# Kernel optimization log

Hardware: AMD Instinct MI355X
Metric: run time of the kernel (lower is better)

The kernel has to match this reference:

```python
import jax, jax.numpy as jnp
import numpy as np

D = 85  # label-distribution length -> selects A3 branch

def _build_A(d):
    if d == 5:
        base = jnp.arange(5)
        return 1.0 - jnp.abs(base[:, None] - base[None, :]) / 5.0
    if d == 10:
        base = jnp.arange(10)
        return 1.0 - jnp.abs(base[:, None] - base[None, :]) / 10.0
    base = jnp.arange(85)
    return (1.0 - jnp.abs(base[:, None] - base[None, :]) / 85.0).astype(jnp.float32)

def setup_inputs() -> dict:
    key = jax.random.key(0)
    k1, k2 = jax.random.split(key)
    B = 262144
    inp = jax.random.normal(k1, (B, D), dtype=jnp.float32)
    tgt = jax.random.uniform(k2, (B, D), dtype=jnp.float32)
    return {"input": inp, "target": tgt}

def reference(input, target):
    A = _build_A(input.shape[1]).astype(input.dtype)
    diff = jnp.abs(input - target)            # [B, d]
    # per-row quadratic form diff_i^T A diff_i, summed over batch
    q = jnp.einsum('bi,ij,bj->b', diff, A, diff)
    return 0.1 * q.sum()
```

## Files before the change

kernel.cpp:

```cpp
#include <hip/hip_runtime.h>
#include <hip/hip_bf16.h>


#define QFD_D 85
#define ROWS_PER_BLOCK 128
#define THREADS 256

__global__ __launch_bounds__(THREADS) void qfd_kernel(
    const float* __restrict__ in, const float* __restrict__ tgt,
    float* __restrict__ out) {
    __shared__ float diff[ROWS_PER_BLOCK * QFD_D];
    __shared__ float wsum[THREADS / 64];

    const int tid = threadIdx.x;
    const int E = ROWS_PER_BLOCK * QFD_D;
    const int base = blockIdx.x * E;

    const float4* in4 = reinterpret_cast<const float4*>(in + base);
    const float4* tg4 = reinterpret_cast<const float4*>(tgt + base);
    float4* df4 = reinterpret_cast<float4*>(diff);
    for (int idx = tid; idx < E / 4; idx += THREADS) {
        float4 a = in4[idx];
        float4 b = tg4[idx];
        float4 r;
        r.x = fabsf(a.x - b.x);
        r.y = fabsf(a.y - b.y);
        r.z = fabsf(a.z - b.z);
        r.w = fabsf(a.w - b.w);
        df4[idx] = r;
    }
    __syncthreads();

    float q = 0.0f;
    if (tid < ROWS_PER_BLOCK) {
        const float* d = &diff[tid * QFD_D];
        float L = 0.0f, sumL = 0.0f, sumL2 = 0.0f;
        #pragma unroll 4
        for (int k = 0; k < QFD_D - 1; ++k) {
            L += d[k];
            sumL += L;
            sumL2 = fmaf(L, L, sumL2);
        }
        const float S = L + d[QFD_D - 1];
        q = fmaf(S, S, -(2.0f / 85.0f) * (S * sumL - sumL2));
    }

    #pragma unroll
    for (int off = 32; off > 0; off >>= 1)
        q += __shfl_down(q, off, 64);
    if ((tid & 63) == 0) wsum[tid >> 6] = q;
    __syncthreads();
    if (tid == 0) {
        float s = 0.0f;
        #pragma unroll
        for (int w = 0; w < THREADS / 64; ++w) s += wsum[w];
        atomicAdd(out, 0.1f * s);
    }
}

extern "C" void kernel_launch(void* const* d_in, const int* in_sizes, int n_in,
                              void* d_out, int out_size, void* d_ws, size_t ws_size,
                              hipStream_t stream) {
    const float* in  = (const float*)d_in[0];
    const float* tgt = (const float*)d_in[1];
    float* out = (float*)d_out;

    const int B = in_sizes[0] / QFD_D;
    const int grid = B / ROWS_PER_BLOCK;

    hipMemsetAsync(d_out, 0, sizeof(float), stream);
    qfd_kernel<<<grid, THREADS, 0, stream>>>(in, tgt, out);
}
```

Measured before the change: 198.0 us.

## Process four rows per thread from registers and reduce partials in a second kernel

Each thread now streams four consecutive rows (85 float4 loads) straight into registers and computes the prefix-sum quadratic form in place, with no shared-memory staging or block barrier. The single global atomic and the memset are replaced by per-block partial sums written to the workspace, followed by a one-block reduction kernel. The goal is to drop LDS traffic and idle threads. The cost is strided per-thread float4 loads: adjacent lanes are 1360 bytes apart, so coalescing is poor, and the fully unrolled loop adds register pressure plus a second launch.

```diff
diff --git a/kernel.cpp b/kernel.cpp
--- a/kernel.cpp
+++ b/kernel.cpp
@@ -3,58 +3,64 @@
 
 
 #define QFD_D 85
-#define ROWS_PER_BLOCK 128
-#define THREADS 256
+#define THREADS 128
 
 __global__ __launch_bounds__(THREADS) void qfd_kernel(
     const float* __restrict__ in, const float* __restrict__ tgt,
-    float* __restrict__ out) {
-    __shared__ float diff[ROWS_PER_BLOCK * QFD_D];
-    __shared__ float wsum[THREADS / 64];
+    float* __restrict__ partial) {
+    const int tid = blockIdx.x * THREADS + threadIdx.x;
+    const float4* in4 = reinterpret_cast<const float4*>(in)  + tid * QFD_D;
+    const float4* tg4 = reinterpret_cast<const float4*>(tgt) + tid * QFD_D;
 
-    const int tid = threadIdx.x;
-    const int E = ROWS_PER_BLOCK * QFD_D;
-    const int base = blockIdx.x * E;
-
-    const float4* in4 = reinterpret_cast<const float4*>(in + base);
-    const float4* tg4 = reinterpret_cast<const float4*>(tgt + base);
-    float4* df4 = reinterpret_cast<float4*>(diff);
-    for (int idx = tid; idx < E / 4; idx += THREADS) {
-        float4 a = in4[idx];
-        float4 b = tg4[idx];
-        float4 r;
-        r.x = fabsf(a.x - b.x);
-        r.y = fabsf(a.y - b.y);
-        r.z = fabsf(a.z - b.z);
-        r.w = fabsf(a.w - b.w);
-        df4[idx] = r;
-    }
-    __syncthreads();
-
-    float q = 0.0f;
-    if (tid < ROWS_PER_BLOCK) {
-        const float* d = &diff[tid * QFD_D];
-        float L = 0.0f, sumL = 0.0f, sumL2 = 0.0f;
-        #pragma unroll 4
-        for (int k = 0; k < QFD_D - 1; ++k) {
-            L += d[k];
-            sumL += L;
-            sumL2 = fmaf(L, L, sumL2);
+    float l = 0.0f, a1 = 0.0f, b2 = 0.0f, qs = 0.0f;
+    #pragma unroll
+    for (int j = 0; j < 85; ++j) {
+        float4 a = in4[j];
+        float4 b = tg4[j];
+        float e[4] = {a.x - b.x, a.y - b.y, a.z - b.z, a.w - b.w};
+        #pragma unroll
+        for (int c = 0; c < 4; ++c) {
+            float v = fabsf(e[c]);
+            l += v;
+            a1 += l;
+            b2 = fmaf(l, l, b2);
+            if (((4 * j + c) % QFD_D) == QFD_D - 1) {
+                float S = l;
+                float sumL  = a1 - S;
+                float sumL2 = fmaf(-S, S, b2);
+                qs += fmaf(S, S, -(2.0f / 85.0f) * (S * sumL - sumL2));
+                l = 0.0f; a1 = 0.0f; b2 = 0.0f;
+            }
         }
-        const float S = L + d[QFD_D - 1];
-        q = fmaf(S, S, -(2.0f / 85.0f) * (S * sumL - sumL2));
     }
 
     #pragma unroll
-    for (int off = 32; off > 0; off >>= 1)
-        q += __shfl_down(q, off, 64);
-    if ((tid & 63) == 0) wsum[tid >> 6] = q;
+    for (int m = 32; m > 0; m >>= 1)
+        qs += __shfl_xor(qs, m, 64);
+    __shared__ float ws[THREADS / 64];
+    const int lane = threadIdx.x & 63;
+    const int wave = threadIdx.x >> 6;
+    if (lane == 0) ws[wave] = qs;
+    __syncthreads();
+    if (threadIdx.x == 0) partial[blockIdx.x] = ws[0] + ws[1];
+}
+
+__global__ __launch_bounds__(256) void qfd_reduce_kernel(
+    const float* __restrict__ partial, float* __restrict__ out, int n) {
+    __shared__ float wsum[4];
+    const int tid = threadIdx.x;
+    float s = 0.0f;
+    for (int i = tid; i < n; i += 256) s += partial[i];
+    #pragma unroll
+    for (int m = 32; m > 0; m >>= 1)
+        s += __shfl_xor(s, m, 64);
+    if ((tid & 63) == 0) wsum[tid >> 6] = s;
     __syncthreads();
     if (tid == 0) {
-        float s = 0.0f;
+        float t = 0.0f;
         #pragma unroll
-        for (int w = 0; w < THREADS / 64; ++w) s += wsum[w];
-        atomicAdd(out, 0.1f * s);
+        for (int w = 0; w < 4; ++w) t += wsum[w];
+        out[0] = 0.1f * t;
     }
 }
 
@@ -64,10 +70,12 @@
     const float* in  = (const float*)d_in[0];
     const float* tgt = (const float*)d_in[1];
     float* out = (float*)d_out;
+    float* partial = (float*)d_ws;
 
     const int B = in_sizes[0] / QFD_D;
-    const int grid = B / ROWS_PER_BLOCK;
+    const int groups = B / 4;
+    const int grid = groups / THREADS;
 
-    hipMemsetAsync(d_out, 0, sizeof(float), stream);
-    qfd_kernel<<<grid, THREADS, 0, stream>>>(in, tgt, out);
+    qfd_kernel<<<grid, THREADS, 0, stream>>>(in, tgt, partial);
+    qfd_reduce_kernel<<<1, 256, 0, stream>>>(partial, out, grid);
 }
```

New measurement: 212.9 us. +7.5%, slower.
